# Performance work log

Hardware: AMD Instinct MI355X
Metric: run time of the kernel (lower is better)

Reference implementation:

```python
import jax, jax.numpy as jnp
import numpy as np

H = 2048      # hidden_dim
DI = 4096     # intermediate_size
N = 128       # state_size
NH = 64       # num_heads
P = 64        # head_dim
K = 4         # conv kernel
CH = 256      # chunk size
L = 4096      # seq len
DT_MIN, DT_MAX = 1e-3, 1e2


def setup_inputs() -> dict:
    key = jax.random.key(0)
    ks = jax.random.split(key, 8)
    conv_dim = DI + 2 * N
    x = jax.random.normal(ks[0], (L, H), jnp.float32)
    W_in = jax.random.normal(ks[1], (DI + 2 * N + NH, H), jnp.float32) / np.sqrt(H)
    conv_w = jax.random.normal(ks[2], (conv_dim, 1, K), jnp.float32) / np.sqrt(K)
    conv_b = jax.random.normal(ks[3], (conv_dim,), jnp.float32) * 0.01
    u = jax.random.uniform(ks[4], (NH,))
    dt = jnp.exp(u * (np.log(0.1) - np.log(0.001)) + np.log(0.001))
    dt = jnp.maximum(dt, 1e-4)
    dt_bias = dt + jnp.log(-jnp.expm1(-dt))   # inverse-softplus init
    A_log = jnp.log(jax.random.uniform(ks[5], (NH,), minval=1.0, maxval=16.0))
    D = jnp.ones((NH,), jnp.float32)
    norm_w = jnp.ones((DI,), jnp.float32)
    W_out = jax.random.normal(ks[6], (H, DI), jnp.float32) / np.sqrt(DI)
    return dict(x=x, W_in=W_in, conv_w=conv_w, conv_b=conv_b, dt_bias=dt_bias,
                A_log=A_log, D=D, norm_w=norm_w, W_out=W_out)


def _causal_decay(a):
    # a: [..., T] per-step log-decays -> exp(segment sum) as lower-tri [..., T, T]
    T = a.shape[-1]
    strict = jnp.tril(jnp.ones((T, T), bool), -1)
    full = jnp.tril(jnp.ones((T, T), bool), 0)
    s = jnp.cumsum(jnp.where(strict, a[..., None], 0.0), axis=-2)
    return jnp.where(full, jnp.exp(s), 0.0)


def reference(x, W_in, conv_w, conv_b, dt_bias, A_log, D, norm_w, W_out):
    conv_dim = DI + 2 * N
    xBCdt = x @ W_in.T                                  # [L, DI+2N+NH]
    xBC, dt = xBCdt[:, :conv_dim], xBCdt[:, conv_dim:]
    # causal depthwise conv1d + SiLU
    z = jax.lax.conv_general_dilated(
        xBC.T[None], conv_w, (1,), [(K - 1, 0)],
        dimension_numbers=('NCH', 'OIH', 'NCH'),
        feature_group_count=conv_dim)[0] + conv_b[:, None]
    xBC = jax.nn.silu(z.T)                              # [L, conv_dim]
    x_ssm = xBC[:, :DI].reshape(L, NH, P)
    Bm = xBC[:, DI:DI + N]                              # [L, N] shared over heads
    Cm = xBC[:, DI + N:]                                # [L, N]
    dt = jnp.clip(jax.nn.softplus(dt + dt_bias), DT_MIN, DT_MAX)  # [L, NH]
    A = -jnp.exp(A_log.astype(jnp.float32))             # [NH]
    dA = dt * A                                         # [L, NH]
    xdt = x_ssm * dt[:, :, None]                        # [L, NH, P]
    nc = L // CH
    xc = xdt.reshape(nc, CH, NH, P)
    Bc = Bm.reshape(nc, CH, N)
    Cc = Cm.reshape(nc, CH, N)
    dAc = dA.reshape(nc, CH, NH)
    A_cs = jnp.cumsum(dAc, axis=1)                      # [c, k, h]
    # intra-chunk (diagonal blocks)
    Lmat = _causal_decay(dAc.transpose(0, 2, 1))        # [c, h, k, k]
    Y_diag = jnp.einsum('ckn,csn,chks,cshp->ckhp', Cc, Bc, Lmat, xc)
    # per-chunk right states
    decay_states = jnp.exp(A_cs[:, -1:, :] - A_cs)      # [c, k, h]
    states = jnp.einsum('ckn,ckh,ckhp->chpn', Bc, decay_states, xc)
    # inter-chunk recurrence (no initial state)
    chunk_sum = A_cs[:, -1, :].T                        # [h, c]
    dec = _causal_decay(jnp.pad(chunk_sum, ((0, 0), (1, 0))))  # [h, c+1, c+1]
    states = jnp.concatenate([jnp.zeros((1, NH, P, N), states.dtype), states], 0)
    new_states = jnp.einsum('hzc,chpn->zhpn', dec, states)      # [c+1, h, p, n]
    prev = new_states[:-1]                              # [c, h, p, n]
    Y_off = jnp.einsum('ckn,chpn,ckh->ckhp', Cc, prev, jnp.exp(A_cs))
    Y = (Y_diag + Y_off).reshape(L, NH, P) + x_ssm * D[None, :, None]
    y = Y.reshape(L, DI)
    # RMSNorm
    var = jnp.mean(jnp.square(y.astype(jnp.float32)), -1, keepdims=True)
    y = (y * jax.lax.rsqrt(var + 1e-6)) * norm_w
    return y @ W_out.T
```

## Files before the change

kernel.cpp:

```cpp
#include <hip/hip_runtime.h>


typedef __bf16 bf16;
typedef __bf16 bf16x8 __attribute__((ext_vector_type(8)));
typedef __bf16 bf16x4 __attribute__((ext_vector_type(4)));
typedef float  f32x4  __attribute__((ext_vector_type(4)));

#define DEV static __device__ __forceinline__

DEV f32x4 mfma16(bf16x8 a, bf16x8 b, f32x4 c) {
  return __builtin_amdgcn_mfma_f32_16x16x32_bf16(a, b, c, 0, 0, 0);
}

DEV void gll16(const bf16* g, bf16* l) {
  __builtin_amdgcn_global_load_lds(
      (const __attribute__((address_space(1))) unsigned int*)g,
      (__attribute__((address_space(3))) unsigned int*)l, 16, 0, 0);
}

#define BAR()   asm volatile("s_barrier" ::: "memory")
#define VMW(n)  asm volatile("s_waitcnt vmcnt(" #n ")" ::: "memory")

template <int NT, int LD, bool DTC>
__global__ __launch_bounds__(512) void gemm_kernel(
    const bf16* __restrict__ Abase, const bf16* __restrict__ Bbase,
    bf16* __restrict__ C0, bf16* __restrict__ C1,
    float* __restrict__ dt0, float* __restrict__ dt1, int ldc, int ntN) {
  __shared__ __align__(16) bf16 lds[3 * 16384];
  const int tid = threadIdx.x;
  const int wid = tid >> 6, lane = tid & 63;
  const int lrow = lane & 15;
  const int lc = lane >> 4;
  const int wm = wid & 1, wn = wid >> 1;
  const int bx = blockIdx.x / ntN, by = blockIdx.x % ntN;
  const int row0 = bx * 256, col0 = by * 256;
  const bf16* A = Abase + (size_t)blockIdx.y * (NT * 32);
  const bf16* B = Bbase + (size_t)blockIdx.y * (NT * 32);
  bf16* C = blockIdx.y ? C1 : C0;

  const bf16* gA[2];
  const bf16* gB[2];
#pragma unroll
  for (int q = 0; q < 2; ++q) {
    int P = q * 8192 + tid * 16;
    int Bq = P ^ (((P >> 7) & 3) << 4);
    int srow = Bq >> 6;
    int selem = (Bq & 63) >> 1;
    gA[q] = A + (size_t)(row0 + srow) * LD + selem;
    gB[q] = B + (size_t)(col0 + srow) * LD + selem;
  }
  auto stage = [&](int s, int ko) {
    bf16* sl = lds + s * 16384;
    gll16(gA[0] + ko, sl + tid * 8);
    gll16(gA[1] + ko, sl + 4096 + tid * 8);
    gll16(gB[0] + ko, sl + 8192 + tid * 8);
    gll16(gB[1] + ko, sl + 12288 + tid * 8);
  };
  auto rdA = [&](int s, int m) -> bf16x8 {
    int row = wm * 128 + m * 16 + lrow;
    int off = row * 64 + ((lc ^ ((row >> 1) & 3)) << 4);
    return *(const bf16x8*)((const char*)(lds + s * 16384) + off);
  };
  auto rdB = [&](int s, int n) -> bf16x8 {
    int row = wn * 64 + n * 16 + lrow;
    int off = row * 64 + ((lc ^ ((row >> 1) & 3)) << 4);
    return *(const bf16x8*)((const char*)(lds + s * 16384) + 16384 + off);
  };

  f32x4 acc[8][4] = {};
  stage(0, 0);
  stage(1, 32);
  int rs = 0, ws = 2;
  for (int t = 0; t < NT; ++t) {
    if (t + 1 < NT) { VMW(4); } else { VMW(0); }
    BAR();
    if (t + 2 < NT) stage(ws, (t + 2) * 32);
    bf16x8 b0 = rdB(rs, 0), b1 = rdB(rs, 1), b2 = rdB(rs, 2), b3 = rdB(rs, 3);
#pragma unroll
    for (int m = 0; m < 8; ++m) {
      bf16x8 a = rdA(rs, m);
      acc[m][0] = mfma16(a, b0, acc[m][0]);
      acc[m][1] = mfma16(a, b1, acc[m][1]);
      acc[m][2] = mfma16(a, b2, acc[m][2]);
      acc[m][3] = mfma16(a, b3, acc[m][3]);
    }
    rs = (rs == 2) ? 0 : rs + 1;
    ws = (ws == 2) ? 0 : ws + 1;
  }
  const int orow = lc * 4;
#pragma unroll
  for (int m = 0; m < 8; ++m)
#pragma unroll
    for (int n = 0; n < 4; ++n)
#pragma unroll
      for (int i = 0; i < 4; ++i) {
        int r = row0 + wm * 128 + m * 16 + orow + i;
        int c = col0 + wn * 64 + n * 16 + lrow;
        C[(size_t)r * ldc + c] = (bf16)acc[m][n][i];
      }
  if (DTC && by == 17 && wn == 0) {
    float* dtp = blockIdx.y ? dt1 : dt0;
#pragma unroll
    for (int m = 0; m < 8; ++m)
#pragma unroll
      for (int n = 0; n < 4; ++n)
#pragma unroll
        for (int i = 0; i < 4; ++i) {
          int r = row0 + wm * 128 + m * 16 + orow + i;
          int h = n * 16 + lrow;
          dtp[(size_t)r * 64 + h] = acc[m][n][i];
        }
  }
}

__global__ __launch_bounds__(256) void add2b_kernel(
    const bf16* __restrict__ a, const bf16* __restrict__ b,
    float* __restrict__ o, long n8) {
  long i = (long)blockIdx.x * blockDim.x + threadIdx.x;
  long stride = (long)gridDim.x * blockDim.x;
  for (; i < n8; i += stride) {
    bf16x8 va = ((const bf16x8*)a)[i];
    bf16x8 vb = ((const bf16x8*)b)[i];
    float4 o0, o1;
    o0.x = (float)va[0] + (float)vb[0];
    o0.y = (float)va[1] + (float)vb[1];
    o0.z = (float)va[2] + (float)vb[2];
    o0.w = (float)va[3] + (float)vb[3];
    o1.x = (float)va[4] + (float)vb[4];
    o1.y = (float)va[5] + (float)vb[5];
    o1.z = (float)va[6] + (float)vb[6];
    o1.w = (float)va[7] + (float)vb[7];
    ((float4*)o)[i * 2] = o0;
    ((float4*)o)[i * 2 + 1] = o1;
  }
}

__global__ __launch_bounds__(256) void cast_f2b_kernel(
    const float* __restrict__ in, bf16* __restrict__ out, long n4) {
  long i = (long)blockIdx.x * blockDim.x + threadIdx.x;
  long stride = (long)gridDim.x * blockDim.x;
  for (; i < n4; i += stride) {
    float4 v = ((const float4*)in)[i];
    bf16x4 o = {(bf16)v.x, (bf16)v.y, (bf16)v.z, (bf16)v.w};
    ((bf16x4*)out)[i] = o;
  }
}

__global__ __launch_bounds__(256) void cast_pad_kernel(
    const float* __restrict__ in, bf16* __restrict__ out, long n4, long valid4) {
  long i = (long)blockIdx.x * blockDim.x + threadIdx.x;
  long stride = (long)gridDim.x * blockDim.x;
  for (; i < n4; i += stride) {
    bf16x4 o = {(bf16)0.f, (bf16)0.f, (bf16)0.f, (bf16)0.f};
    if (i < valid4) {
      float4 v = ((const float4*)in)[i];
      o = bf16x4{(bf16)v.x, (bf16)v.y, (bf16)v.z, (bf16)v.w};
    }
    ((bf16x4*)out)[i] = o;
  }
}

__global__ __launch_bounds__(256) void dt_scan_kernel(
    const float* __restrict__ dt0, const float* __restrict__ dt1,
    const float* __restrict__ dt_bias, const float* __restrict__ A_log,
    float* __restrict__ dt, float* __restrict__ Acs, float* __restrict__ decayO,
    float* __restrict__ expAcs, float* __restrict__ csum) {
  const int c = blockIdx.x, h = blockIdx.y;
  const int k = threadIdx.x;
  const int t = c * 256 + k;
  __shared__ float buf[256];
  size_t idx = (size_t)t * 64 + h;
  float raw = dt0[idx] + dt1[idx] + dt_bias[h];
  float dtv = raw > 20.f ? raw : log1pf(__expf(raw));
  dtv = fminf(fmaxf(dtv, 0.001f), 100.f);
  dt[(size_t)t * 64 + h] = dtv;
  float dA = -__expf(A_log[h]) * dtv;
  buf[k] = dA;
  __syncthreads();
  for (int off = 1; off < 256; off <<= 1) {
    float add = (k >= off) ? buf[k - off] : 0.f;
    __syncthreads();
    buf[k] += add;
    __syncthreads();
  }
  float v = buf[k];
  float total = buf[255];
  size_t base = (size_t)(c * 64 + h) * 256 + k;
  Acs[base] = v;
  expAcs[base] = __expf(v);
  decayO[base] = __expf(total - v);
  if (k == 0) csum[c * 64 + h] = total;
}

__global__ __launch_bounds__(256) void conv_kernel(
    const bf16* __restrict__ xp0, const bf16* __restrict__ xp1,
    const float* __restrict__ conv_w, const float* __restrict__ conv_b,
    const float* __restrict__ dt, bf16* __restrict__ XS,
    bf16* __restrict__ XDT_T, bf16* __restrict__ Bm, bf16* __restrict__ BT,
    bf16* __restrict__ Cm) {
  const int t0 = blockIdx.x * 64;
  const int c0 = blockIdx.y * 64;
  __shared__ float lin[67 * 64];
  __shared__ bf16 tr[64 * 72];
  const int tid = threadIdx.x;
  for (int idx = tid; idx < 67 * 64; idx += 256) {
    int r = idx >> 6, cc = idx & 63;
    int gt = t0 + r - 3;
    size_t g = (size_t)gt * 4608 + c0 + cc;
    lin[idx] = (gt >= 0) ? ((float)xp0[g] + (float)xp1[g]) : 0.f;
  }
  __syncthreads();
  const int cl = tid & 63, tg = tid >> 6;
  const int ch = c0 + cl;
  const float w0 = conv_w[ch * 4 + 0], w1 = conv_w[ch * 4 + 1];
  const float w2 = conv_w[ch * 4 + 2], w3 = conv_w[ch * 4 + 3];
  const float bb = conv_b[ch];
  float vals[16];
  for (int j = 0; j < 16; ++j) {
    int tl = tg * 16 + j;
    float s = bb + lin[tl * 64 + cl] * w0 + lin[(tl + 1) * 64 + cl] * w1 +
              lin[(tl + 2) * 64 + cl] * w2 + lin[(tl + 3) * 64 + cl] * w3;
    vals[j] = s / (1.f + __expf(-s));
  }
  if (c0 < 4096) {
    const int hh = c0 >> 6;
    for (int j = 0; j < 16; ++j) {
      int t = t0 + tg * 16 + j;
      XS[(size_t)t * 4096 + ch] = (bf16)vals[j];
    }
    __syncthreads();
    for (int j = 0; j < 16; ++j) {
      int tl = tg * 16 + j;
      float dtv = dt[(size_t)(t0 + tl) * 64 + hh];
      tr[cl * 72 + tl] = (bf16)(vals[j] * dtv);
    }
    __syncthreads();
    int p = tid >> 2, toff = (tid & 3) * 16;
    bf16* dst = XDT_T + (size_t)(hh * 64 + p) * 4096 + t0 + toff;
    *(bf16x8*)(dst) = *(const bf16x8*)(tr + p * 72 + toff);
    *(bf16x8*)(dst + 8) = *(const bf16x8*)(tr + p * 72 + toff + 8);
  } else if (c0 < 4224) {
    const int n0 = c0 - 4096;
    for (int j = 0; j < 16; ++j) {
      int t = t0 + tg * 16 + j;
      Bm[(size_t)t * 128 + n0 + cl] = (bf16)vals[j];
    }
    __syncthreads();
    for (int j = 0; j < 16; ++j) tr[cl * 72 + tg * 16 + j] = (bf16)vals[j];
    __syncthreads();
    int p = tid >> 2, toff = (tid & 3) * 16;
    bf16* dst = BT + (size_t)(n0 + p) * 4096 + t0 + toff;
    *(bf16x8*)(dst) = *(const bf16x8*)(tr + p * 72 + toff);
    *(bf16x8*)(dst + 8) = *(const bf16x8*)(tr + p * 72 + toff + 8);
  } else {
    const int n0 = c0 - 4224;
    for (int j = 0; j < 16; ++j) {
      int t = t0 + tg * 16 + j;
      Cm[(size_t)t * 128 + n0 + cl] = (bf16)vals[j];
    }
  }
}

__global__ __launch_bounds__(256) void gmat_kernel(
    const bf16* __restrict__ Cm, const bf16* __restrict__ Bm,
    bf16* __restrict__ G) {
  const int c = blockIdx.x, kt = blockIdx.y, st = blockIdx.z;
  const int tid = threadIdx.x;
  const int wave = tid >> 6, lane = tid & 63;
  const int lrow = lane & 15, lk = (lane >> 4) * 8;
  const int wr = (wave >> 1) * 64, wc = (wave & 1) * 64;
  f32x4 acc[4][4] = {};
  for (int kk = 0; kk < 4; ++kk) {
    bf16x8 aF[4], bF[4];
    for (int m = 0; m < 4; ++m)
      aF[m] = *(const bf16x8*)(Cm + (size_t)(c * 256 + kt * 128 + wr + m * 16 + lrow) * 128 + kk * 32 + lk);
    for (int n = 0; n < 4; ++n)
      bF[n] = *(const bf16x8*)(Bm + (size_t)(c * 256 + st * 128 + wc + n * 16 + lrow) * 128 + kk * 32 + lk);
    for (int m = 0; m < 4; ++m)
      for (int n = 0; n < 4; ++n)
        acc[m][n] = mfma16(aF[m], bF[n], acc[m][n]);
  }
  const int orow = (lane >> 4) * 4;
  for (int m = 0; m < 4; ++m)
    for (int n = 0; n < 4; ++n)
      for (int i = 0; i < 4; ++i) {
        int k = kt * 128 + wr + m * 16 + orow + i;
        int s = st * 128 + wc + n * 16 + lrow;
        G[((size_t)c * 256 + k) * 256 + s] = (bf16)acc[m][n][i];
      }
}

__global__ __launch_bounds__(256) void states_kernel(
    const bf16* __restrict__ XDT_T, const bf16* __restrict__ BT,
    const float* __restrict__ decayO, float* __restrict__ states) {
  const int c = blockIdx.x, h = blockIdx.y;
  __shared__ bf16 Ap[64 * 264];
  __shared__ float sDec[256];
  const int tid = threadIdx.x;
  const int wave = tid >> 6, lane = tid & 63;
  const int lrow = lane & 15, lk = (lane >> 4) * 8;
  sDec[tid] = decayO[(size_t)(c * 64 + h) * 256 + tid];
  __syncthreads();
  {
    int p = tid >> 2, kb = (tid & 3) * 64;
    const bf16* src = XDT_T + (size_t)(h * 64 + p) * 4096 + c * 256 + kb;
    for (int j = 0; j < 8; ++j) {
      bf16x8 v = *(const bf16x8*)(src + j * 8);
      bf16x8 o;
      for (int i = 0; i < 8; ++i) o[i] = (bf16)((float)v[i] * sDec[kb + j * 8 + i]);
      *(bf16x8*)(Ap + p * 264 + kb + j * 8) = o;
    }
  }
  __syncthreads();
  const int nb = wave * 32;
  f32x4 acc[4][2] = {};
  for (int kk = 0; kk < 8; ++kk) {
    bf16x8 aF[4], bF[2];
    for (int m = 0; m < 4; ++m)
      aF[m] = *(const bf16x8*)(Ap + (m * 16 + lrow) * 264 + kk * 32 + lk);
    for (int n = 0; n < 2; ++n)
      bF[n] = *(const bf16x8*)(BT + (size_t)(nb + n * 16 + lrow) * 4096 + c * 256 + kk * 32 + lk);
    for (int m = 0; m < 4; ++m)
      for (int n = 0; n < 2; ++n)
        acc[m][n] = mfma16(aF[m], bF[n], acc[m][n]);
  }
  float* st = states + (size_t)(c * 64 + h) * 64 * 128;
  const int orow = (lane >> 4) * 4;
  for (int m = 0; m < 4; ++m)
    for (int n = 0; n < 2; ++n)
      for (int i = 0; i < 4; ++i)
        st[(size_t)(m * 16 + orow + i) * 128 + nb + n * 16 + lrow] = acc[m][n][i];
}

__global__ __launch_bounds__(128) void chunk_rec_kernel(
    const float* __restrict__ states, const float* __restrict__ csum,
    bf16* __restrict__ prev) {
  const int h = blockIdx.x, p = blockIdx.y;
  const int n = threadIdx.x;
  size_t base = (size_t)h * 64 * 128 + (size_t)p * 128 + n;
  float run = 0.f;
  for (int c = 0; c < 16; ++c) {
    size_t idx = (size_t)c * 64 * 64 * 128 + base;
    prev[idx] = (bf16)run;
    run = run * __expf(csum[c * 64 + h]) + states[idx];
  }
}

__global__ __launch_bounds__(256) void ydiag_kernel(
    const bf16* __restrict__ Cm, const bf16* __restrict__ prev,
    const bf16* __restrict__ Gb, const float* __restrict__ Acs,
    const float* __restrict__ expAcs, const bf16* __restrict__ XDT_T,
    float* __restrict__ Y) {
  const int c = blockIdx.x, h = blockIdx.y;
  __shared__ float sAcs[256];
  __shared__ float sExp[256];
  __shared__ __align__(16) bf16 pv[64 * 136];
  __shared__ __align__(16) bf16 xd[64 * 264];
  const int tid = threadIdx.x;
  const int wave = tid >> 6, lane = tid & 63;
  const int lrow = lane & 15, lk = (lane >> 4) * 8;
  const int wv16 = wave * 16;
  sAcs[tid] = Acs[(size_t)(c * 64 + h) * 256 + tid];
  sExp[tid] = expAcs[(size_t)(c * 64 + h) * 256 + tid];
  {
    int r = tid >> 2, q = (tid & 3) * 32;
    const bf16* src = prev + (size_t)(c * 64 + h) * 8192 + r * 128 + q;
    bf16* dst = pv + r * 136 + q;
    for (int j = 0; j < 4; ++j)
      *(bf16x8*)(dst + j * 8) = *(const bf16x8*)(src + j * 8);
  }
  {
    int r = tid >> 2, q = (tid & 3) * 64;
    const bf16* src = XDT_T + (size_t)(h * 64 + r) * 4096 + c * 256 + q;
    bf16* dst = xd + r * 264 + q;
    for (int j = 0; j < 8; ++j)
      *(bf16x8*)(dst + j * 8) = *(const bf16x8*)(src + j * 8);
  }
  __syncthreads();
  f32x4 acc[4][4] = {};
  bf16x8 aYo[4][4];
#pragma unroll
  for (int kk = 0; kk < 4; ++kk)
#pragma unroll
    for (int m = 0; m < 4; ++m)
      aYo[kk][m] = *(const bf16x8*)(Cm + (size_t)(c * 256 + m * 64 + wv16 + lrow) * 128 + kk * 32 + lk);
#pragma unroll
  for (int kk = 0; kk < 4; ++kk) {
    bf16x8 bF[4];
#pragma unroll
    for (int n = 0; n < 4; ++n)
      bF[n] = *(const bf16x8*)(pv + (n * 16 + lrow) * 136 + kk * 32 + lk);
#pragma unroll
    for (int m = 0; m < 4; ++m)
#pragma unroll
      for (int n = 0; n < 4; ++n)
        acc[m][n] = mfma16(aYo[kk][m], bF[n], acc[m][n]);
  }
  const int orow = (lane >> 4) * 4;
#pragma unroll
  for (int m = 0; m < 4; ++m)
#pragma unroll
    for (int i = 0; i < 4; ++i) {
      float e = sExp[m * 64 + wv16 + orow + i];
      for (int n = 0; n < 4; ++n) acc[m][n][i] *= e;
    }
  const bf16* Gp = Gb + (size_t)c * 65536;
#pragma unroll
  for (int stile = 0; stile < 4; ++stile) {
    const int s0 = stile * 64;
    bf16x8 graw[2][4];
#pragma unroll
    for (int kk = 0; kk < 2; ++kk)
#pragma unroll
      for (int m = 0; m < 4; ++m)
        if (m * 64 + wv16 + 15 >= s0) {
          int row = m * 64 + wv16 + lrow;
          graw[kk][m] = *(const bf16x8*)(Gp + (size_t)row * 256 + s0 + kk * 32 + lk);
        }
    bf16x8 bF[2][4];
#pragma unroll
    for (int kk = 0; kk < 2; ++kk)
#pragma unroll
      for (int n = 0; n < 4; ++n)
        bF[kk][n] = *(const bf16x8*)(xd + (n * 16 + lrow) * 264 + s0 + kk * 32 + lk);
#pragma unroll
    for (int kk = 0; kk < 2; ++kk)
#pragma unroll
      for (int m = 0; m < 4; ++m) {
        if (m * 64 + wv16 + 15 < s0) continue;
        const int row = m * 64 + wv16 + lrow;
        const float ak = sAcs[row];
        bf16x8 af;
#pragma unroll
        for (int j = 0; j < 8; ++j) {
          int s = s0 + kk * 32 + lk + j;
          float v = (float)graw[kk][m][j] * __expf(ak - sAcs[s]);
          if (s > row) v = 0.f;
          af[j] = (bf16)v;
        }
#pragma unroll
        for (int n = 0; n < 4; ++n)
          acc[m][n] = mfma16(af, bF[kk][n], acc[m][n]);
      }
  }
#pragma unroll
  for (int m = 0; m < 4; ++m)
#pragma unroll
    for (int n = 0; n < 4; ++n)
#pragma unroll
      for (int i = 0; i < 4; ++i) {
        int t = c * 256 + m * 64 + wv16 + orow + i;
        int col = h * 64 + n * 16 + lrow;
        Y[(size_t)t * 4096 + col] = acc[m][n][i];
      }
}

__global__ __launch_bounds__(256) void rmsnorm_kernel(
    const float* __restrict__ Y, const bf16* __restrict__ XS,
    const float* __restrict__ Dp, const float* __restrict__ norm_w,
    bf16* __restrict__ out) {
  const int row = blockIdx.x;
  const float4* y4 = (const float4*)(Y + (size_t)row * 4096);
  const bf16x4* xs4 = (const bf16x4*)(XS + (size_t)row * 4096);
  float4 v[4];
  float ss = 0.f;
  for (int j = 0; j < 4; ++j) {
    int c4 = threadIdx.x + j * 256;
    float4 y = y4[c4];
    bf16x4 xs = xs4[c4];
    float d = Dp[(c4 * 4) >> 6];
    y.x += (float)xs[0] * d;
    y.y += (float)xs[1] * d;
    y.z += (float)xs[2] * d;
    y.w += (float)xs[3] * d;
    v[j] = y;
    ss += y.x * y.x + y.y * y.y + y.z * y.z + y.w * y.w;
  }
  for (int off = 32; off; off >>= 1) ss += __shfl_down(ss, off, 64);
  __shared__ float ws[4];
  if ((threadIdx.x & 63) == 0) ws[threadIdx.x >> 6] = ss;
  __syncthreads();
  float scale = rsqrtf((ws[0] + ws[1] + ws[2] + ws[3]) / 4096.f + 1e-6f);
  for (int j = 0; j < 4; ++j) {
    int col = (threadIdx.x + j * 256) * 4;
    float4 w = *(const float4*)(norm_w + col);
    bf16x4 o = {(bf16)(v[j].x * scale * w.x), (bf16)(v[j].y * scale * w.y),
                (bf16)(v[j].z * scale * w.z), (bf16)(v[j].w * scale * w.w)};
    *(bf16x4*)(out + (size_t)row * 4096 + col) = o;
  }
}

extern "C" void kernel_launch(void* const* d_in, const int* in_sizes, int n_in,
                              void* d_out, int out_size, void* d_ws, size_t ws_size,
                              hipStream_t stream) {
  const float* x       = (const float*)d_in[0];
  const float* W_in    = (const float*)d_in[1];
  const float* conv_w  = (const float*)d_in[2];
  const float* conv_b  = (const float*)d_in[3];
  const float* dt_bias = (const float*)d_in[4];
  const float* A_log   = (const float*)d_in[5];
  const float* Dp      = (const float*)d_in[6];
  const float* norm_w  = (const float*)d_in[7];
  const float* W_out   = (const float*)d_in[8];

  size_t o = 0;
  char* base = (char*)d_ws;
  auto take = [&](size_t b) {
    char* p = base + o;
    o += (b + 255) & ~(size_t)255;
    return (void*)p;
  };
  bf16*  xb     = (bf16*)take((size_t)4096 * 2048 * 2);
  bf16*  winb   = (bf16*)take((size_t)4608 * 2048 * 2);
  bf16*  xp0b   = (bf16*)take((size_t)4096 * 4608 * 2);
  bf16*  xp1b   = (bf16*)take((size_t)4096 * 4608 * 2);
  float* dt0    = (float*)take((size_t)4096 * 64 * 4);
  float* dt1    = (float*)take((size_t)4096 * 64 * 4);
  float* dtg    = (float*)take((size_t)4096 * 64 * 4);
  float* Acs    = (float*)take((size_t)4096 * 64 * 4);
  float* decayO = (float*)take((size_t)4096 * 64 * 4);
  float* expA   = (float*)take((size_t)4096 * 64 * 4);
  float* csum   = (float*)take((size_t)16 * 64 * 4);
  bf16*  XS     = (bf16*)take((size_t)4096 * 4096 * 2);
  bf16*  XDT_T  = (bf16*)take((size_t)4096 * 4096 * 2);
  bf16*  Bm     = (bf16*)take((size_t)4096 * 128 * 2);
  bf16*  BT     = (bf16*)take((size_t)4096 * 128 * 2);
  bf16*  Cm     = (bf16*)take((size_t)4096 * 128 * 2);
  float* Y      = (float*)take((size_t)4096 * 4096 * 4);
  bf16*  Gb     = (bf16*)((char*)xp0b);
  float* states = (float*)((char*)xp0b + (size_t)4194304);
  bf16*  prev   = (bf16*)((char*)xp0b + (size_t)37748736);
  bf16*  woutb  = (bf16*)((char*)xp0b + (size_t)54525952);
  bf16*  ynorm  = xb;
  bf16*  p2a    = XS;
  bf16*  p2b    = XDT_T;

  cast_f2b_kernel<<<2048, 256, 0, stream>>>(x, xb, (long)4096 * 2048 / 4);
  cast_pad_kernel<<<2048, 256, 0, stream>>>(W_in, winb, (long)4608 * 2048 / 4,
                                            (long)4416 * 2048 / 4);
  gemm_kernel<32, 2048, true><<<dim3(288, 2), 512, 0, stream>>>(
      xb, winb, xp0b, xp1b, dt0, dt1, 4608, 18);
  dt_scan_kernel<<<dim3(16, 64), 256, 0, stream>>>(dt0, dt1, dt_bias, A_log,
                                                   dtg, Acs, decayO, expA, csum);
  conv_kernel<<<dim3(64, 68), 256, 0, stream>>>(xp0b, xp1b, conv_w, conv_b, dtg,
                                                XS, XDT_T, Bm, BT, Cm);
  gmat_kernel<<<dim3(16, 2, 2), 256, 0, stream>>>(Cm, Bm, Gb);
  states_kernel<<<dim3(16, 64), 256, 0, stream>>>(XDT_T, BT, decayO, states);
  chunk_rec_kernel<<<dim3(64, 64), 128, 0, stream>>>(states, csum, prev);
  cast_f2b_kernel<<<2048, 256, 0, stream>>>(W_out, woutb, (long)2048 * 4096 / 4);
  ydiag_kernel<<<dim3(16, 64), 256, 0, stream>>>(Cm, prev, Gb, Acs, expA,
                                                 XDT_T, Y);
  rmsnorm_kernel<<<4096, 256, 0, stream>>>(Y, XS, Dp, norm_w, ynorm);
  gemm_kernel<64, 4096, false><<<dim3(128, 2), 512, 0, stream>>>(
      ynorm, woutb, p2a, p2b, nullptr, nullptr, 2048, 8);
  add2b_kernel<<<2048, 256, 0, stream>>>(p2a, p2b, (float*)d_out,
                                         (long)4096 * 2048 / 8);
}
```

Before: 345.7 us.

## Drop split-K on input GEMM, shrink GEMM tile to 256x128, emit fp32

The GEMM tile changes from 256x256 to 256x128 with 4x2 warps, which shrinks LDS use and accumulators and adds an occupancy hint of 4 blocks. The input projection no longer splits K in two with bf16 partials. It now runs the full K in one pass and writes a single fp32 xBCdt buffer, which dt_scan and conv read directly. This removes the separate dt partial buffers and the summing of two partials. The cost is more fp32 output traffic and lower data reuse per tile.

New measurement: 352.4 us. Within noise of the previous version (+1.9%).

```diff
diff --git a/kernel.cpp b/kernel.cpp
--- a/kernel.cpp
+++ b/kernel.cpp
@@ -21,63 +21,67 @@
 #define BAR()   asm volatile("s_barrier" ::: "memory")
 #define VMW(n)  asm volatile("s_waitcnt vmcnt(" #n ")" ::: "memory")
 
-template <int NT, int LD, bool DTC>
-__global__ __launch_bounds__(512) void gemm_kernel(
+template <int NT, int LD, bool F32OUT>
+__global__ __launch_bounds__(512, 4) void gemm_kernel(
     const bf16* __restrict__ Abase, const bf16* __restrict__ Bbase,
-    bf16* __restrict__ C0, bf16* __restrict__ C1,
-    float* __restrict__ dt0, float* __restrict__ dt1, int ldc, int ntN) {
-  __shared__ __align__(16) bf16 lds[3 * 16384];
+    float* __restrict__ Cf, bf16* __restrict__ Cb0, bf16* __restrict__ Cb1,
+    int ldc, int ntN) {
+  __shared__ __align__(16) bf16 lds[3 * 12288];
   const int tid = threadIdx.x;
   const int wid = tid >> 6, lane = tid & 63;
   const int lrow = lane & 15;
   const int lc = lane >> 4;
-  const int wm = wid & 1, wn = wid >> 1;
+  const int wm = wid & 3, wn = wid >> 2;
   const int bx = blockIdx.x / ntN, by = blockIdx.x % ntN;
-  const int row0 = bx * 256, col0 = by * 256;
+  const int row0 = bx * 256, col0 = by * 128;
   const bf16* A = Abase + (size_t)blockIdx.y * (NT * 32);
   const bf16* B = Bbase + (size_t)blockIdx.y * (NT * 32);
-  bf16* C = blockIdx.y ? C1 : C0;
 
   const bf16* gA[2];
-  const bf16* gB[2];
+  const bf16* gB0;
 #pragma unroll
   for (int q = 0; q < 2; ++q) {
     int P = q * 8192 + tid * 16;
-    int Bq = P ^ (((P >> 7) & 3) << 4);
-    int srow = Bq >> 6;
-    int selem = (Bq & 63) >> 1;
+    int Lq = P ^ (((P >> 7) & 3) << 4);
+    int srow = Lq >> 6;
+    int selem = (Lq & 63) >> 1;
     gA[q] = A + (size_t)(row0 + srow) * LD + selem;
-    gB[q] = B + (size_t)(col0 + srow) * LD + selem;
+  }
+  {
+    int P = tid * 16;
+    int Lq = P ^ (((P >> 7) & 3) << 4);
+    int srow = Lq >> 6;
+    int selem = (Lq & 63) >> 1;
+    gB0 = B + (size_t)(col0 + srow) * LD + selem;
   }
   auto stage = [&](int s, int ko) {
-    bf16* sl = lds + s * 16384;
+    bf16* sl = lds + s * 12288;
     gll16(gA[0] + ko, sl + tid * 8);
     gll16(gA[1] + ko, sl + 4096 + tid * 8);
-    gll16(gB[0] + ko, sl + 8192 + tid * 8);
-    gll16(gB[1] + ko, sl + 12288 + tid * 8);
+    gll16(gB0 + ko, sl + 8192 + tid * 8);
   };
   auto rdA = [&](int s, int m) -> bf16x8 {
-    int row = wm * 128 + m * 16 + lrow;
+    int row = wm * 64 + m * 16 + lrow;
     int off = row * 64 + ((lc ^ ((row >> 1) & 3)) << 4);
-    return *(const bf16x8*)((const char*)(lds + s * 16384) + off);
+    return *(const bf16x8*)((const char*)lds + s * 24576 + off);
   };
   auto rdB = [&](int s, int n) -> bf16x8 {
     int row = wn * 64 + n * 16 + lrow;
     int off = row * 64 + ((lc ^ ((row >> 1) & 3)) << 4);
-    return *(const bf16x8*)((const char*)(lds + s * 16384) + 16384 + off);
+    return *(const bf16x8*)((const char*)lds + s * 24576 + 16384 + off);
   };
 
-  f32x4 acc[8][4] = {};
+  f32x4 acc[4][4] = {};
   stage(0, 0);
   stage(1, 32);
   int rs = 0, ws = 2;
   for (int t = 0; t < NT; ++t) {
-    if (t + 1 < NT) { VMW(4); } else { VMW(0); }
+    if (t + 1 < NT) { VMW(3); } else { VMW(0); }
     BAR();
     if (t + 2 < NT) stage(ws, (t + 2) * 32);
     bf16x8 b0 = rdB(rs, 0), b1 = rdB(rs, 1), b2 = rdB(rs, 2), b3 = rdB(rs, 3);
 #pragma unroll
-    for (int m = 0; m < 8; ++m) {
+    for (int m = 0; m < 4; ++m) {
       bf16x8 a = rdA(rs, m);
       acc[m][0] = mfma16(a, b0, acc[m][0]);
       acc[m][1] = mfma16(a, b1, acc[m][1]);
@@ -88,27 +92,28 @@
     ws = (ws == 2) ? 0 : ws + 1;
   }
   const int orow = lc * 4;
-#pragma unroll
-  for (int m = 0; m < 8; ++m)
-#pragma unroll
-    for (int n = 0; n < 4; ++n)
-#pragma unroll
-      for (int i = 0; i < 4; ++i) {
-        int r = row0 + wm * 128 + m * 16 + orow + i;
-        int c = col0 + wn * 64 + n * 16 + lrow;
-        C[(size_t)r * ldc + c] = (bf16)acc[m][n][i];
-      }
-  if (DTC && by == 17 && wn == 0) {
-    float* dtp = blockIdx.y ? dt1 : dt0;
-#pragma unroll
-    for (int m = 0; m < 8; ++m)
+  if (F32OUT) {
+#pragma unroll
+    for (int m = 0; m < 4; ++m)
 #pragma unroll
       for (int n = 0; n < 4; ++n)
 #pragma unroll
         for (int i = 0; i < 4; ++i) {
-          int r = row0 + wm * 128 + m * 16 + orow + i;
-          int h = n * 16 + lrow;
-          dtp[(size_t)r * 64 + h] = acc[m][n][i];
+          int r = row0 + wm * 64 + m * 16 + orow + i;
+          int c = col0 + wn * 64 + n * 16 + lrow;
+          Cf[(size_t)r * ldc + c] = acc[m][n][i];
+        }
+  } else {
+    bf16* C = blockIdx.y ? Cb1 : Cb0;
+#pragma unroll
+    for (int m = 0; m < 4; ++m)
+#pragma unroll
+      for (int n = 0; n < 4; ++n)
+#pragma unroll
+        for (int i = 0; i < 4; ++i) {
+          int r = row0 + wm * 64 + m * 16 + orow + i;
+          int c = col0 + wn * 64 + n * 16 + lrow;
+          C[(size_t)r * ldc + c] = (bf16)acc[m][n][i];
         }
   }
 }
@@ -161,16 +166,15 @@
 }
 
 __global__ __launch_bounds__(256) void dt_scan_kernel(
-    const float* __restrict__ dt0, const float* __restrict__ dt1,
-    const float* __restrict__ dt_bias, const float* __restrict__ A_log,
-    float* __restrict__ dt, float* __restrict__ Acs, float* __restrict__ decayO,
+    const float* __restrict__ xBCdt, const float* __restrict__ dt_bias,
+    const float* __restrict__ A_log, float* __restrict__ dt,
+    float* __restrict__ Acs, float* __restrict__ decayO,
     float* __restrict__ expAcs, float* __restrict__ csum) {
   const int c = blockIdx.x, h = blockIdx.y;
   const int k = threadIdx.x;
   const int t = c * 256 + k;
   __shared__ float buf[256];
-  size_t idx = (size_t)t * 64 + h;
-  float raw = dt0[idx] + dt1[idx] + dt_bias[h];
+  float raw = xBCdt[(size_t)t * 4608 + 4352 + h] + dt_bias[h];
   float dtv = raw > 20.f ? raw : log1pf(__expf(raw));
   dtv = fminf(fmaxf(dtv, 0.001f), 100.f);
   dt[(size_t)t * 64 + h] = dtv;
@@ -193,11 +197,10 @@
 }
 
 __global__ __launch_bounds__(256) void conv_kernel(
-    const bf16* __restrict__ xp0, const bf16* __restrict__ xp1,
-    const float* __restrict__ conv_w, const float* __restrict__ conv_b,
-    const float* __restrict__ dt, bf16* __restrict__ XS,
-    bf16* __restrict__ XDT_T, bf16* __restrict__ Bm, bf16* __restrict__ BT,
-    bf16* __restrict__ Cm) {
+    const float* __restrict__ xBCdt, const float* __restrict__ conv_w,
+    const float* __restrict__ conv_b, const float* __restrict__ dt,
+    bf16* __restrict__ XS, bf16* __restrict__ XDT_T, bf16* __restrict__ Bm,
+    bf16* __restrict__ BT, bf16* __restrict__ Cm) {
   const int t0 = blockIdx.x * 64;
   const int c0 = blockIdx.y * 64;
   __shared__ float lin[67 * 64];
@@ -206,8 +209,7 @@
   for (int idx = tid; idx < 67 * 64; idx += 256) {
     int r = idx >> 6, cc = idx & 63;
     int gt = t0 + r - 3;
-    size_t g = (size_t)gt * 4608 + c0 + cc;
-    lin[idx] = (gt >= 0) ? ((float)xp0[g] + (float)xp1[g]) : 0.f;
+    lin[idx] = (gt >= 0) ? xBCdt[(size_t)gt * 4608 + c0 + cc] : 0.f;
   }
   __syncthreads();
   const int cl = tid & 63, tg = tid >> 6;
@@ -512,10 +514,7 @@
   };
   bf16*  xb     = (bf16*)take((size_t)4096 * 2048 * 2);
   bf16*  winb   = (bf16*)take((size_t)4608 * 2048 * 2);
-  bf16*  xp0b   = (bf16*)take((size_t)4096 * 4608 * 2);
-  bf16*  xp1b   = (bf16*)take((size_t)4096 * 4608 * 2);
-  float* dt0    = (float*)take((size_t)4096 * 64 * 4);
-  float* dt1    = (float*)take((size_t)4096 * 64 * 4);
+  float* xBCdt  = (float*)take((size_t)4096 * 4608 * 4);
   float* dtg    = (float*)take((size_t)4096 * 64 * 4);
   float* Acs    = (float*)take((size_t)4096 * 64 * 4);
   float* decayO = (float*)take((size_t)4096 * 64 * 4);
@@ -527,10 +526,10 @@
   bf16*  BT     = (bf16*)take((size_t)4096 * 128 * 2);
   bf16*  Cm     = (bf16*)take((size_t)4096 * 128 * 2);
   float* Y      = (float*)take((size_t)4096 * 4096 * 4);
-  bf16*  Gb     = (bf16*)((char*)xp0b);
-  float* states = (float*)((char*)xp0b + (size_t)4194304);
-  bf16*  prev   = (bf16*)((char*)xp0b + (size_t)37748736);
-  bf16*  woutb  = (bf16*)((char*)xp0b + (size_t)54525952);
+  bf16*  Gb     = (bf16*)((char*)xBCdt);
+  float* states = (float*)((char*)xBCdt + (size_t)4194304);
+  bf16*  prev   = (bf16*)((char*)xBCdt + (size_t)37748736);
+  bf16*  woutb  = (bf16*)((char*)xBCdt + (size_t)54525952);
   bf16*  ynorm  = xb;
   bf16*  p2a    = XS;
   bf16*  p2b    = XDT_T;
@@ -538,12 +537,12 @@
   cast_f2b_kernel<<<2048, 256, 0, stream>>>(x, xb, (long)4096 * 2048 / 4);
   cast_pad_kernel<<<2048, 256, 0, stream>>>(W_in, winb, (long)4608 * 2048 / 4,
                                             (long)4416 * 2048 / 4);
-  gemm_kernel<32, 2048, true><<<dim3(288, 2), 512, 0, stream>>>(
-      xb, winb, xp0b, xp1b, dt0, dt1, 4608, 18);
-  dt_scan_kernel<<<dim3(16, 64), 256, 0, stream>>>(dt0, dt1, dt_bias, A_log,
-                                                   dtg, Acs, decayO, expA, csum);
-  conv_kernel<<<dim3(64, 68), 256, 0, stream>>>(xp0b, xp1b, conv_w, conv_b, dtg,
-                                                XS, XDT_T, Bm, BT, Cm);
+  gemm_kernel<64, 2048, true><<<dim3(576, 1), 512, 0, stream>>>(
+      xb, winb, xBCdt, nullptr, nullptr, 4608, 36);
+  dt_scan_kernel<<<dim3(16, 64), 256, 0, stream>>>(xBCdt, dt_bias, A_log, dtg,
+                                                   Acs, decayO, expA, csum);
+  conv_kernel<<<dim3(64, 68), 256, 0, stream>>>(xBCdt, conv_w, conv_b, dtg, XS,
+                                                XDT_T, Bm, BT, Cm);
   gmat_kernel<<<dim3(16, 2, 2), 256, 0, stream>>>(Cm, Bm, Gb);
   states_kernel<<<dim3(16, 64), 256, 0, stream>>>(XDT_T, BT, decayO, states);
   chunk_rec_kernel<<<dim3(64, 64), 128, 0, stream>>>(states, csum, prev);
@@ -551,8 +550,8 @@
   ydiag_kernel<<<dim3(16, 64), 256, 0, stream>>>(Cm, prev, Gb, Acs, expA,
                                                  XDT_T, Y);
   rmsnorm_kernel<<<4096, 256, 0, stream>>>(Y, XS, Dp, norm_w, ynorm);
-  gemm_kernel<64, 4096, false><<<dim3(128, 2), 512, 0, stream>>>(
-      ynorm, woutb, p2a, p2b, nullptr, nullptr, 2048, 8);
+  gemm_kernel<64, 4096, false><<<dim3(256, 2), 512, 0, stream>>>(
+      ynorm, woutb, nullptr, p2a, p2b, 2048, 16);
   add2b_kernel<<<2048, 256, 0, stream>>>(p2a, p2b, (float*)d_out,
                                          (long)4096 * 2048 / 8);
 }
```
